# Performance work log

Hardware: AMD Instinct MI355X
Metric: run time of the kernel (lower is better)

## Reference

```python
import jax, jax.numpy as jnp
import numpy as np

N = 50000
IN_C, HID_C, OUT_C = 128, 64, 32
E = 800000
NEG_SLOPE = 0.2


def setup_inputs() -> dict:
    key = jax.random.key(0)
    ks = jax.random.split(key, 8)
    x = jax.random.normal(ks[0], (N, IN_C), dtype=jnp.float32)
    edge_index = jax.random.randint(ks[1], (2, E), 0, N, dtype=jnp.int64)
    # GATConv params (heads=1): lin weight, att_src/att_dst vectors, bias
    sc = 1.0 / np.sqrt(IN_C)
    W = jax.random.uniform(ks[2], (IN_C, HID_C), jnp.float32, -sc, sc)
    att_src = jax.random.normal(ks[3], (HID_C,), jnp.float32) * (1.0 / np.sqrt(HID_C))
    att_dst = jax.random.normal(ks[4], (HID_C,), jnp.float32) * (1.0 / np.sqrt(HID_C))
    bias_conv = jnp.zeros((HID_C,), jnp.float32)
    sl = 1.0 / np.sqrt(HID_C)
    W_lin = jax.random.uniform(ks[5], (HID_C, OUT_C), jnp.float32, -sl, sl)
    b_lin = jax.random.uniform(ks[6], (OUT_C,), jnp.float32, -sl, sl)
    return {"x": x, "edge_index": edge_index, "W": W, "att_src": att_src,
            "att_dst": att_dst, "bias_conv": bias_conv, "W_lin": W_lin, "b_lin": b_lin}


def reference(x, edge_index, W, att_src, att_dst, bias_conv, W_lin, b_lin):
    n = x.shape[0]
    h = x @ W  # [N, HID]
    # add self-loops (PyG GATConv default add_self_loops=True)
    loop = jnp.arange(n, dtype=edge_index.dtype)
    src = jnp.concatenate([edge_index[0], loop])  # [E+N]
    dst = jnp.concatenate([edge_index[1], loop])
    a_src = h @ att_src  # [N]
    a_dst = h @ att_dst
    e = jax.nn.leaky_relu(a_src[src] + a_dst[dst], NEG_SLOPE)  # [E+N]
    # segment softmax over incoming edges per destination node
    m = jax.ops.segment_max(e, dst, num_segments=n)
    e = jnp.exp(e - m[dst])
    denom = jax.ops.segment_sum(e, dst, num_segments=n)
    alpha = e / (denom[dst] + 1e-16)
    msg = alpha[:, None] * h[src]  # [E+N, HID]
    out = jax.ops.segment_sum(msg, dst, num_segments=n) + bias_conv
    out = jax.nn.relu(out)
    return out @ W_lin + b_lin
```

## Files before the change

### kernel.cpp

```cpp
#include <hip/hip_runtime.h>
#include <hip/hip_bf16.h>

#define IN_C  128
#define HID_C 64
#define OUT_C 32
#define NEG_SLOPE 0.2f
#define EPB1    2048
#define EPB2    2048
#define BUCKETW 64
#define RCAP    1536
#define SUPW    1024
#define RCAP1   18432
#define PARTS   9
#define CSTRIDE 16
#define XS_LD   136

typedef short bf16x8 __attribute__((ext_vector_type(8)));
typedef float f32x4  __attribute__((ext_vector_type(4)));

__device__ __forceinline__ unsigned short f2bf(float f) {
    __hip_bfloat16 h = __float2bfloat16(f);
    return *(unsigned short*)&h;
}
__device__ __forceinline__ float bflo(unsigned int u) {
    return __uint_as_float(u << 16);
}
__device__ __forceinline__ float bfhi(unsigned int u) {
    return __uint_as_float(u & 0xffff0000u);
}

__global__ __launch_bounds__(256) void gemm_bin1_kernel(
    const float* __restrict__ x, const float* __restrict__ W,
    const float* __restrict__ att_src, const float* __restrict__ att_dst,
    __hip_bfloat16* __restrict__ hb,
    float* __restrict__ a_src, float* __restrict__ a_dst,
    const int* __restrict__ ei, int E,
    int* __restrict__ bcur1, unsigned* __restrict__ superbuf,
    int ngemm, int n_nodes)
{
    __shared__ __align__(16) unsigned char smem[8960];
    const int t = threadIdx.x;

    if ((int)blockIdx.x < ngemm) {
        unsigned short* xs = (unsigned short*)smem;
        float (*redA)[16] = (float(*)[16])(smem + 4352);
        float (*redD)[16] = (float(*)[16])(smem + 4608);
        const int wv   = t >> 6;
        const int lane = t & 63;
        const int m16  = lane & 15;
        const int quad = lane >> 4;
        const int node0 = blockIdx.x * 16;
        const int nrows = min(16, n_nodes - node0);

        const int ncol = wv * 16 + m16;
        bf16x8 B[4];
#pragma unroll
        for (int k0 = 0; k0 < 4; ++k0)
#pragma unroll
            for (int j = 0; j < 8; ++j)
                B[k0][j] = (short)f2bf(W[(k0 * 32 + quad * 8 + j) * HID_C + ncol]);

        {
            const float4* xg = (const float4*)(x + (long)node0 * IN_C);
#pragma unroll
            for (int i = t; i < 512; i += 256) {
                const int row = i >> 5;
                const int c4  = i & 31;
                float4 v = (row < nrows) ? xg[i] : make_float4(0.f, 0.f, 0.f, 0.f);
                ushort4 u;
                u.x = f2bf(v.x); u.y = f2bf(v.y);
                u.z = f2bf(v.z); u.w = f2bf(v.w);
                *(ushort4*)(xs + row * XS_LD + c4 * 4) = u;
            }
        }
        __syncthreads();

        f32x4 C = {0.f, 0.f, 0.f, 0.f};
#pragma unroll
        for (int k0 = 0; k0 < 4; ++k0) {
            const bf16x8 A = *(const bf16x8*)(xs + m16 * XS_LD + k0 * 32 + quad * 8);
            C = __builtin_amdgcn_mfma_f32_16x16x32_bf16(A, B[k0], C, 0, 0, 0);
        }

#pragma unroll
        for (int r = 0; r < 4; ++r) {
            const int row = quad * 4 + r;
            if (row < nrows)
                hb[(long)(node0 + row) * HID_C + ncol] = __float2bfloat16(C[r]);
        }

        {
            const float av = att_src[ncol];
            const float dv = att_dst[ncol];
            float ps[4], pd[4];
#pragma unroll
            for (int r = 0; r < 4; ++r) { ps[r] = C[r] * av; pd[r] = C[r] * dv; }
#pragma unroll
            for (int off = 1; off <= 8; off <<= 1) {
#pragma unroll
                for (int r = 0; r < 4; ++r) {
                    ps[r] += __shfl_xor(ps[r], off, 64);
                    pd[r] += __shfl_xor(pd[r], off, 64);
                }
            }
            if (m16 == 0) {
#pragma unroll
                for (int r = 0; r < 4; ++r) {
                    redA[wv][quad * 4 + r] = ps[r];
                    redD[wv][quad * 4 + r] = pd[r];
                }
            }
        }
        __syncthreads();
        if (t < 16 && t < nrows) {
            a_src[node0 + t] = redA[0][t] + redA[1][t] + redA[2][t] + redA[3][t];
            a_dst[node0 + t] = redD[0][t] + redD[1][t] + redD[2][t] + redD[3][t];
        }
    } else {
        unsigned* stage = (unsigned*)smem;
        int* excl = (int*)(smem + 8192);
        int* cur  = (int*)(smem + 8448);
        int* gpos = (int*)(smem + 8704);

        const int base = (blockIdx.x - ngemm) * EPB1;
        const int nedge = min(EPB1, E - base);

        if (t < 64) excl[t] = 0;
        __syncthreads();

        for (int i = t; i < nedge; i += 256)
            atomicAdd(&excl[ei[E + base + i] >> 10], 1);
        __syncthreads();

        if (t < 64) {
            int c = excl[t], incl = c;
#pragma unroll
            for (int off = 1; off <= 32; off <<= 1) {
                int u = __shfl_up(incl, off, 64);
                if (t >= off) incl += u;
            }
            excl[t] = incl - c;
            cur[t]  = incl - c;
        }
        __syncthreads();

        for (int i = t; i < nedge; i += 256) {
            const int s = ei[base + i];
            const int d = ei[E + base + i];
            const int sq = d >> 10;
            const int pos = atomicAdd(&cur[sq], 1);
            stage[pos] = (unsigned)s | ((unsigned)(d & 1023) << 16)
                         | ((unsigned)sq << 26);
        }
        __syncthreads();

        if (t < 64) {
            const int c = cur[t] - excl[t];
            gpos[t] = (c > 0) ? atomicAdd(&bcur1[t * CSTRIDE], c) : 0;
        }
        __syncthreads();

        for (int i = t; i < nedge; i += 256) {
            const unsigned r = stage[i];
            const int sq = r >> 26;
            const int dp = gpos[sq] + (i - excl[sq]);
            if (dp < RCAP1) superbuf[(long)sq * RCAP1 + dp] = r;
        }
    }
}

__global__ __launch_bounds__(256) void bin2_kernel(
    const unsigned* __restrict__ superbuf, const int* __restrict__ bcur1,
    int* __restrict__ bcur2, unsigned* __restrict__ bucketbuf)
{
    __shared__ unsigned srt[EPB2];
    __shared__ int cnt[16];
    __shared__ int rp[16];
    __shared__ int cur16[16];
    __shared__ int gpos[16];

    const int t    = threadIdx.x;
    const int sq   = blockIdx.x / PARTS;
    const int part = blockIdx.x % PARTS;
    const int tot  = min(bcur1[sq * CSTRIDE], RCAP1);
    const int beg  = part * EPB2;
    const int n    = min(EPB2, tot - beg);
    if (n <= 0) return;

    if (t < 16) cnt[t] = 0;
    __syncthreads();

    const unsigned* src = superbuf + (long)sq * RCAP1 + beg;

    for (int i = t; i < n; i += 256)
        atomicAdd(&cnt[(src[i] >> 22) & 15], 1);
    __syncthreads();

    if (t == 0) {
        int run = 0;
#pragma unroll
        for (int k = 0; k < 16; ++k) { rp[k] = run; cur16[k] = run; run += cnt[k]; }
    }
    __syncthreads();

    for (int i = t; i < n; i += 256) {
        const unsigned r = src[i];
        const int pos = atomicAdd(&cur16[(r >> 22) & 15], 1);
        srt[pos] = r;
    }
    __syncthreads();

    if (t < 16) {
        const int c = cnt[t];
        const int q2 = sq * 16 + t;
        gpos[t] = (c > 0) ? atomicAdd(&bcur2[q2 * CSTRIDE], c) : 0;
    }
    __syncthreads();

    for (int i = t; i < n; i += 256) {
        const unsigned r = srt[i];
        const int idx = (r >> 22) & 15;
        const int dp  = gpos[idx] + (i - rp[idx]);
        const int q2  = sq * 16 + idx;
        const unsigned nx = (r & 0xFFFFu) | (((r >> 16) & 63u) << 16);
        if (dp < RCAP) bucketbuf[(long)q2 * RCAP + dp] = nx;
    }
}

__global__ __launch_bounds__(512) void bucket_agg_kernel(
    const unsigned* __restrict__ bucketbuf, const int* __restrict__ bcursor,
    const __hip_bfloat16* __restrict__ hb,
    const float* __restrict__ a_src, const float* __restrict__ a_dst,
    const float* __restrict__ bias_conv,
    const float* __restrict__ W_lin, const float* __restrict__ b_lin,
    float* __restrict__ out, int n_nodes)
{
    __shared__ unsigned srtL[RCAP];
    __shared__ int cntd[BUCKETW];
    __shared__ int rp[BUCKETW + 1];
    __shared__ int curd[BUCKETW];

    const int t  = threadIdx.x;
    const int q  = blockIdx.x;
    const int d0 = q * BUCKETW;
    const int dmax = min(BUCKETW, n_nodes - d0);
    const int tot  = min(bcursor[q * CSTRIDE], RCAP);
    const int wv = t >> 6, lane = t & 63, g8 = lane >> 3, l = lane & 7;

    if (t < BUCKETW) cntd[t] = 0;
    __syncthreads();

    const unsigned* gsrc = bucketbuf + (long)q * RCAP;

    for (int i = t; i < tot; i += 512)
        atomicAdd(&cntd[(gsrc[i] >> 16) & 63], 1);
    __syncthreads();

    if (t < 64) {
        int c = cntd[t], incl = c;
#pragma unroll
        for (int off = 1; off <= 32; off <<= 1) {
            int u = __shfl_up(incl, off, 64);
            if (t >= off) incl += u;
        }
        rp[t] = incl - c;
        curd[t] = incl - c;
        if (t == 63) rp[64] = incl;
    }
    __syncthreads();

    for (int i = t; i < tot; i += 512) {
        const unsigned r = gsrc[i];
        const int pos = atomicAdd(&curd[(r >> 16) & 63], 1);
        srtL[pos] = r;
    }
    __syncthreads();

    float Wr[8][4];
#pragma unroll
    for (int kc = 0; kc < 8; ++kc)
#pragma unroll
        for (int kj = 0; kj < 4; ++kj)
            Wr[kc][kj] = W_lin[(l * 8 + kc) * OUT_C + g8 * 4 + kj];
    float biasR[8];
#pragma unroll
    for (int kc = 0; kc < 8; ++kc) biasR[kc] = bias_conv[l * 8 + kc];
    float blinR[4];
#pragma unroll
    for (int kj = 0; kj < 4; ++kj) blinR[kj] = b_lin[g8 * 4 + kj];

    const unsigned short* hbs = (const unsigned short*)hb;

    for (int dloc = wv; dloc < dmax; dloc += 8) {
        const int d = d0 + dloc;
        const float ad = a_dst[d];
        float A[8] = {0.f,0.f,0.f,0.f,0.f,0.f,0.f,0.f};
        float den = 0.f;
        if (g8 == 0) {
            float e = a_src[d] + ad;
            e = (e >= 0.f) ? e : NEG_SLOPE * e;
            const float ws = __expf(e);
            const uint4 hv = *(const uint4*)(hbs + (long)d * HID_C + l * 8);
            den = ws;
            A[0] = ws * bflo(hv.x); A[1] = ws * bfhi(hv.x);
            A[2] = ws * bflo(hv.y); A[3] = ws * bfhi(hv.y);
            A[4] = ws * bflo(hv.z); A[5] = ws * bfhi(hv.z);
            A[6] = ws * bflo(hv.w); A[7] = ws * bfhi(hv.w);
        }
        const int beg = rp[dloc], fin = rp[dloc + 1];
        for (int j = beg + g8; j < fin; j += 16) {
            const int  j1   = j + 8;
            const bool has1 = j1 < fin;
            const unsigned r0 = srtL[j];
            const unsigned r1 = srtL[has1 ? j1 : j];
            const int   s0 = r0 & 0xFFFF;
            const int   s1 = r1 & 0xFFFF;
            const float as0 = a_src[s0];
            const float as1 = a_src[s1];
            const uint4 h0 = *(const uint4*)(hbs + (long)s0 * HID_C + l * 8);
            const uint4 h1 = *(const uint4*)(hbs + (long)s1 * HID_C + l * 8);
            float e0 = as0 + ad; e0 = (e0 >= 0.f) ? e0 : NEG_SLOPE * e0;
            float e1 = as1 + ad; e1 = (e1 >= 0.f) ? e1 : NEG_SLOPE * e1;
            const float w0 = __expf(e0);
            const float w1 = has1 ? __expf(e1) : 0.f;
            den += w0 + w1;
            A[0] = fmaf(w0, bflo(h0.x), A[0]); A[1] = fmaf(w0, bfhi(h0.x), A[1]);
            A[2] = fmaf(w0, bflo(h0.y), A[2]); A[3] = fmaf(w0, bfhi(h0.y), A[3]);
            A[4] = fmaf(w0, bflo(h0.z), A[4]); A[5] = fmaf(w0, bfhi(h0.z), A[5]);
            A[6] = fmaf(w0, bflo(h0.w), A[6]); A[7] = fmaf(w0, bfhi(h0.w), A[7]);
            A[0] = fmaf(w1, bflo(h1.x), A[0]); A[1] = fmaf(w1, bfhi(h1.x), A[1]);
            A[2] = fmaf(w1, bflo(h1.y), A[2]); A[3] = fmaf(w1, bfhi(h1.y), A[3]);
            A[4] = fmaf(w1, bflo(h1.z), A[4]); A[5] = fmaf(w1, bfhi(h1.z), A[5]);
            A[6] = fmaf(w1, bflo(h1.w), A[6]); A[7] = fmaf(w1, bfhi(h1.w), A[7]);
        }
#pragma unroll
        for (int off = 8; off <= 32; off <<= 1) {
#pragma unroll
            for (int k = 0; k < 8; ++k) A[k] += __shfl_xor(A[k], off, 64);
            den += __shfl_xor(den, off, 64);
        }
        const float rd = 1.0f / (den + 1e-16f);
        float p0 = 0.f, p1 = 0.f, p2 = 0.f, p3 = 0.f;
#pragma unroll
        for (int kc = 0; kc < 8; ++kc) {
            float vv = fmaf(A[kc], rd, biasR[kc]);
            vv = vv > 0.f ? vv : 0.f;
            p0 = fmaf(vv, Wr[kc][0], p0);
            p1 = fmaf(vv, Wr[kc][1], p1);
            p2 = fmaf(vv, Wr[kc][2], p2);
            p3 = fmaf(vv, Wr[kc][3], p3);
        }
#pragma unroll
        for (int off = 1; off <= 4; off <<= 1) {
            p0 += __shfl_xor(p0, off, 64);
            p1 += __shfl_xor(p1, off, 64);
            p2 += __shfl_xor(p2, off, 64);
            p3 += __shfl_xor(p3, off, 64);
        }
        if (l == 0) {
            float4 o = make_float4(p0 + blinR[0], p1 + blinR[1],
                                   p2 + blinR[2], p3 + blinR[3]);
            *(float4*)(out + (long)d * OUT_C + g8 * 4) = o;
        }
    }
}

extern "C" void kernel_launch(void* const* d_in, const int* in_sizes, int n_in,
                              void* d_out, int out_size, void* d_ws, size_t ws_size,
                              hipStream_t stream) {
    const float* x         = (const float*)d_in[0];
    const int*   ei        = (const int*)d_in[1];
    const float* W         = (const float*)d_in[2];
    const float* att_src   = (const float*)d_in[3];
    const float* att_dst   = (const float*)d_in[4];
    const float* bias_conv = (const float*)d_in[5];
    const float* W_lin     = (const float*)d_in[6];
    const float* b_lin     = (const float*)d_in[7];
    float*       out       = (float*)d_out;

    const int n_nodes = in_sizes[0] / IN_C;
    const int E       = in_sizes[1] / 2;
    const int B1   = (E + EPB1 - 1) / EPB1;
    const int Q    = (n_nodes + BUCKETW - 1) / BUCKETW;
    const int NSUP = (n_nodes + SUPW - 1) / SUPW;
    const int NG   = (n_nodes + 15) / 16;

    __hip_bfloat16* hb = (__hip_bfloat16*)d_ws;
    float* a_src   = (float*)(hb + (long)n_nodes * HID_C);
    float* a_dst   = a_src + n_nodes;
    int*   bcur1   = (int*)(a_dst + n_nodes);
    int*   bcur2   = bcur1 + NSUP * CSTRIDE;
    unsigned* superbuf  = (unsigned*)(bcur2 + (long)Q * CSTRIDE);
    unsigned* bucketbuf = superbuf + (long)NSUP * RCAP1;

    hipMemsetAsync(bcur1, 0,
                   (size_t)(NSUP + Q) * CSTRIDE * sizeof(int), stream);

    gemm_bin1_kernel<<<NG + B1, 256, 0, stream>>>(
        x, W, att_src, att_dst, hb, a_src, a_dst,
        ei, E, bcur1, superbuf, NG, n_nodes);

    bin2_kernel<<<NSUP * PARTS, 256, 0, stream>>>(
        superbuf, bcur1, bcur2, bucketbuf);

    bucket_agg_kernel<<<Q, 512, 0, stream>>>(
        bucketbuf, bcur2, hb, a_src, a_dst,
        bias_conv, W_lin, b_lin, out, n_nodes);
}
```

Measured before the change: 156.0 us.

## Widen GEMM blocks to 64 rows and interleave two destinations in aggregation

The projection GEMM now processes 64 nodes per block, staging a transposed bf16 copy of W in shared memory and computing per-row attention scores within each wave, which removes the cross-wave reduction and a barrier. The aggregation loop handles two destination nodes per wave simultaneously, issuing four gathers per iteration to raise memory-level parallelism. The costs are larger LDS usage, which may reduce occupancy of the binning blocks in the fused kernel, more registers, and wasted iterations when the two edge lists differ in length.

```diff
diff --git a/kernel.cpp b/kernel.cpp
--- a/kernel.cpp
+++ b/kernel.cpp
@@ -38,32 +38,23 @@
     int* __restrict__ bcur1, unsigned* __restrict__ superbuf,
     int ngemm, int n_nodes)
 {
-    __shared__ __align__(16) unsigned char smem[8960];
+    __shared__ __align__(16) unsigned char smem[34816];
     const int t = threadIdx.x;
 
     if ((int)blockIdx.x < ngemm) {
         unsigned short* xs = (unsigned short*)smem;
-        float (*redA)[16] = (float(*)[16])(smem + 4352);
-        float (*redD)[16] = (float(*)[16])(smem + 4608);
+        unsigned short* wt = (unsigned short*)(smem + 17408);
         const int wv   = t >> 6;
         const int lane = t & 63;
         const int m16  = lane & 15;
         const int quad = lane >> 4;
-        const int node0 = blockIdx.x * 16;
-        const int nrows = min(16, n_nodes - node0);
-
-        const int ncol = wv * 16 + m16;
-        bf16x8 B[4];
-#pragma unroll
-        for (int k0 = 0; k0 < 4; ++k0)
-#pragma unroll
-            for (int j = 0; j < 8; ++j)
-                B[k0][j] = (short)f2bf(W[(k0 * 32 + quad * 8 + j) * HID_C + ncol]);
+        const int node0 = blockIdx.x * 64;
+        const int nrows = min(64, n_nodes - node0);
 
         {
             const float4* xg = (const float4*)(x + (long)node0 * IN_C);
 #pragma unroll
-            for (int i = t; i < 512; i += 256) {
+            for (int i = t; i < 2048; i += 256) {
                 const int row = i >> 5;
                 const int c4  = i & 31;
                 float4 v = (row < nrows) ? xg[i] : make_float4(0.f, 0.f, 0.f, 0.f);
@@ -73,28 +64,60 @@
                 *(ushort4*)(xs + row * XS_LD + c4 * 4) = u;
             }
         }
+        {
+#pragma unroll
+            for (int i = t; i < 2048; i += 256) {
+                const int k  = i >> 4;
+                const int n0 = (i & 15) * 4;
+                const float4 v = *(const float4*)(W + k * HID_C + n0);
+                wt[(n0 + 0) * XS_LD + k] = f2bf(v.x);
+                wt[(n0 + 1) * XS_LD + k] = f2bf(v.y);
+                wt[(n0 + 2) * XS_LD + k] = f2bf(v.z);
+                wt[(n0 + 3) * XS_LD + k] = f2bf(v.w);
+            }
+        }
         __syncthreads();
 
-        f32x4 C = {0.f, 0.f, 0.f, 0.f};
-#pragma unroll
-        for (int k0 = 0; k0 < 4; ++k0) {
-            const bf16x8 A = *(const bf16x8*)(xs + m16 * XS_LD + k0 * 32 + quad * 8);
-            C = __builtin_amdgcn_mfma_f32_16x16x32_bf16(A, B[k0], C, 0, 0, 0);
-        }
-
-#pragma unroll
-        for (int r = 0; r < 4; ++r) {
-            const int row = quad * 4 + r;
-            if (row < nrows)
-                hb[(long)(node0 + row) * HID_C + ncol] = __float2bfloat16(C[r]);
+        const int myrow0 = wv * 16;
+        bf16x8 A[4];
+#pragma unroll
+        for (int k0 = 0; k0 < 4; ++k0)
+            A[k0] = *(const bf16x8*)(xs + (myrow0 + m16) * XS_LD + k0 * 32 + quad * 8);
+
+        f32x4 C[4];
+#pragma unroll
+        for (int c = 0; c < 4; ++c) {
+            C[c] = (f32x4){0.f, 0.f, 0.f, 0.f};
+#pragma unroll
+            for (int k0 = 0; k0 < 4; ++k0) {
+                const bf16x8 B = *(const bf16x8*)(wt + (c * 16 + m16) * XS_LD + k0 * 32 + quad * 8);
+                C[c] = __builtin_amdgcn_mfma_f32_16x16x32_bf16(A[k0], B, C[c], 0, 0, 0);
+            }
+        }
+
+#pragma unroll
+        for (int c = 0; c < 4; ++c) {
+#pragma unroll
+            for (int r = 0; r < 4; ++r) {
+                const int row = myrow0 + quad * 4 + r;
+                if (row < nrows)
+                    hb[(long)(node0 + row) * HID_C + c * 16 + m16] = __float2bfloat16(C[c][r]);
+            }
         }
 
         {
-            const float av = att_src[ncol];
-            const float dv = att_dst[ncol];
-            float ps[4], pd[4];
-#pragma unroll
-            for (int r = 0; r < 4; ++r) { ps[r] = C[r] * av; pd[r] = C[r] * dv; }
+            float ps[4] = {0.f, 0.f, 0.f, 0.f};
+            float pd[4] = {0.f, 0.f, 0.f, 0.f};
+#pragma unroll
+            for (int c = 0; c < 4; ++c) {
+                const float av = att_src[c * 16 + m16];
+                const float dv = att_dst[c * 16 + m16];
+#pragma unroll
+                for (int r = 0; r < 4; ++r) {
+                    ps[r] = fmaf(C[c][r], av, ps[r]);
+                    pd[r] = fmaf(C[c][r], dv, pd[r]);
+                }
+            }
 #pragma unroll
             for (int off = 1; off <= 8; off <<= 1) {
 #pragma unroll
@@ -106,15 +129,13 @@
             if (m16 == 0) {
 #pragma unroll
                 for (int r = 0; r < 4; ++r) {
-                    redA[wv][quad * 4 + r] = ps[r];
-                    redD[wv][quad * 4 + r] = pd[r];
+                    const int row = myrow0 + quad * 4 + r;
+                    if (row < nrows) {
+                        a_src[node0 + row] = ps[r];
+                        a_dst[node0 + row] = pd[r];
+                    }
                 }
             }
-        }
-        __syncthreads();
-        if (t < 16 && t < nrows) {
-            a_src[node0 + t] = redA[0][t] + redA[1][t] + redA[2][t] + redA[3][t];
-            a_dst[node0 + t] = redD[0][t] + redD[1][t] + redD[2][t] + redD[3][t];
         }
     } else {
         unsigned* stage = (unsigned*)smem;
@@ -291,76 +312,156 @@
 
     const unsigned short* hbs = (const unsigned short*)hb;
 
-    for (int dloc = wv; dloc < dmax; dloc += 8) {
-        const int d = d0 + dloc;
-        const float ad = a_dst[d];
-        float A[8] = {0.f,0.f,0.f,0.f,0.f,0.f,0.f,0.f};
-        float den = 0.f;
+    for (int p = 0; p < 4; ++p) {
+        const int dA = wv + p * 16;
+        if (dA >= dmax) break;
+        const int dB = dA + 8;
+        const bool vB = dB < dmax;
+        const int gA = d0 + dA;
+        const int gB = d0 + (vB ? dB : dA);
+        const float adA = a_dst[gA];
+        const float adB = a_dst[gB];
+        float Aa[8] = {0.f,0.f,0.f,0.f,0.f,0.f,0.f,0.f};
+        float Ab[8] = {0.f,0.f,0.f,0.f,0.f,0.f,0.f,0.f};
+        float denA = 0.f, denB = 0.f;
+
         if (g8 == 0) {
-            float e = a_src[d] + ad;
-            e = (e >= 0.f) ? e : NEG_SLOPE * e;
-            const float ws = __expf(e);
-            const uint4 hv = *(const uint4*)(hbs + (long)d * HID_C + l * 8);
-            den = ws;
-            A[0] = ws * bflo(hv.x); A[1] = ws * bfhi(hv.x);
-            A[2] = ws * bflo(hv.y); A[3] = ws * bfhi(hv.y);
-            A[4] = ws * bflo(hv.z); A[5] = ws * bfhi(hv.z);
-            A[6] = ws * bflo(hv.w); A[7] = ws * bfhi(hv.w);
-        }
-        const int beg = rp[dloc], fin = rp[dloc + 1];
-        for (int j = beg + g8; j < fin; j += 16) {
-            const int  j1   = j + 8;
-            const bool has1 = j1 < fin;
-            const unsigned r0 = srtL[j];
-            const unsigned r1 = srtL[has1 ? j1 : j];
-            const int   s0 = r0 & 0xFFFF;
-            const int   s1 = r1 & 0xFFFF;
-            const float as0 = a_src[s0];
-            const float as1 = a_src[s1];
-            const uint4 h0 = *(const uint4*)(hbs + (long)s0 * HID_C + l * 8);
-            const uint4 h1 = *(const uint4*)(hbs + (long)s1 * HID_C + l * 8);
-            float e0 = as0 + ad; e0 = (e0 >= 0.f) ? e0 : NEG_SLOPE * e0;
-            float e1 = as1 + ad; e1 = (e1 >= 0.f) ? e1 : NEG_SLOPE * e1;
-            const float w0 = __expf(e0);
-            const float w1 = has1 ? __expf(e1) : 0.f;
-            den += w0 + w1;
-            A[0] = fmaf(w0, bflo(h0.x), A[0]); A[1] = fmaf(w0, bfhi(h0.x), A[1]);
-            A[2] = fmaf(w0, bflo(h0.y), A[2]); A[3] = fmaf(w0, bfhi(h0.y), A[3]);
-            A[4] = fmaf(w0, bflo(h0.z), A[4]); A[5] = fmaf(w0, bfhi(h0.z), A[5]);
-            A[6] = fmaf(w0, bflo(h0.w), A[6]); A[7] = fmaf(w0, bfhi(h0.w), A[7]);
-            A[0] = fmaf(w1, bflo(h1.x), A[0]); A[1] = fmaf(w1, bfhi(h1.x), A[1]);
-            A[2] = fmaf(w1, bflo(h1.y), A[2]); A[3] = fmaf(w1, bfhi(h1.y), A[3]);
-            A[4] = fmaf(w1, bflo(h1.z), A[4]); A[5] = fmaf(w1, bfhi(h1.z), A[5]);
-            A[6] = fmaf(w1, bflo(h1.w), A[6]); A[7] = fmaf(w1, bfhi(h1.w), A[7]);
-        }
+            {
+                float e = a_src[gA] + adA;
+                e = (e >= 0.f) ? e : NEG_SLOPE * e;
+                const float ws = __expf(e);
+                const uint4 hv = *(const uint4*)(hbs + (long)gA * HID_C + l * 8);
+                denA = ws;
+                Aa[0] = ws * bflo(hv.x); Aa[1] = ws * bfhi(hv.x);
+                Aa[2] = ws * bflo(hv.y); Aa[3] = ws * bfhi(hv.y);
+                Aa[4] = ws * bflo(hv.z); Aa[5] = ws * bfhi(hv.z);
+                Aa[6] = ws * bflo(hv.w); Aa[7] = ws * bfhi(hv.w);
+            }
+            if (vB) {
+                float e = a_src[gB] + adB;
+                e = (e >= 0.f) ? e : NEG_SLOPE * e;
+                const float ws = __expf(e);
+                const uint4 hv = *(const uint4*)(hbs + (long)gB * HID_C + l * 8);
+                denB = ws;
+                Ab[0] = ws * bflo(hv.x); Ab[1] = ws * bfhi(hv.x);
+                Ab[2] = ws * bflo(hv.y); Ab[3] = ws * bfhi(hv.y);
+                Ab[4] = ws * bflo(hv.z); Ab[5] = ws * bfhi(hv.z);
+                Ab[6] = ws * bflo(hv.w); Ab[7] = ws * bfhi(hv.w);
+            }
+        }
+
+        const int begA = rp[dA],            finA = rp[dA + 1];
+        const int begB = vB ? rp[dB] : 0;
+        const int finB = vB ? rp[dB + 1] : 0;
+        int jA = begA + g8, jB = begB + g8;
+
+        while ((jA < finA) | (jB < finB)) {
+            const bool hA0 = jA < finA,       hA1 = (jA + 8) < finA;
+            const bool hB0 = jB < finB,       hB1 = (jB + 8) < finB;
+            const unsigned rA0 = srtL[hA0 ? jA       : 0];
+            const unsigned rA1 = srtL[hA1 ? (jA + 8) : 0];
+            const unsigned rB0 = srtL[hB0 ? jB       : 0];
+            const unsigned rB1 = srtL[hB1 ? (jB + 8) : 0];
+            const int sA0 = rA0 & 0xFFFF, sA1 = rA1 & 0xFFFF;
+            const int sB0 = rB0 & 0xFFFF, sB1 = rB1 & 0xFFFF;
+            const float xA0 = a_src[sA0];
+            const float xA1 = a_src[sA1];
+            const float xB0 = a_src[sB0];
+            const float xB1 = a_src[sB1];
+            const uint4 hA0v = *(const uint4*)(hbs + (long)sA0 * HID_C + l * 8);
+            const uint4 hA1v = *(const uint4*)(hbs + (long)sA1 * HID_C + l * 8);
+            const uint4 hB0v = *(const uint4*)(hbs + (long)sB0 * HID_C + l * 8);
+            const uint4 hB1v = *(const uint4*)(hbs + (long)sB1 * HID_C + l * 8);
+            float e0 = xA0 + adA; e0 = (e0 >= 0.f) ? e0 : NEG_SLOPE * e0;
+            float e1 = xA1 + adA; e1 = (e1 >= 0.f) ? e1 : NEG_SLOPE * e1;
+            float e2 = xB0 + adB; e2 = (e2 >= 0.f) ? e2 : NEG_SLOPE * e2;
+            float e3 = xB1 + adB; e3 = (e3 >= 0.f) ? e3 : NEG_SLOPE * e3;
+            const float wA0 = hA0 ? __expf(e0) : 0.f;
+            const float wA1 = hA1 ? __expf(e1) : 0.f;
+            const float wB0 = hB0 ? __expf(e2) : 0.f;
+            const float wB1 = hB1 ? __expf(e3) : 0.f;
+            denA += wA0 + wA1;
+            denB += wB0 + wB1;
+            Aa[0] = fmaf(wA0, bflo(hA0v.x), Aa[0]); Aa[1] = fmaf(wA0, bfhi(hA0v.x), Aa[1]);
+            Aa[2] = fmaf(wA0, bflo(hA0v.y), Aa[2]); Aa[3] = fmaf(wA0, bfhi(hA0v.y), Aa[3]);
+            Aa[4] = fmaf(wA0, bflo(hA0v.z), Aa[4]); Aa[5] = fmaf(wA0, bfhi(hA0v.z), Aa[5]);
+            Aa[6] = fmaf(wA0, bflo(hA0v.w), Aa[6]); Aa[7] = fmaf(wA0, bfhi(hA0v.w), Aa[7]);
+            Aa[0] = fmaf(wA1, bflo(hA1v.x), Aa[0]); Aa[1] = fmaf(wA1, bfhi(hA1v.x), Aa[1]);
+            Aa[2] = fmaf(wA1, bflo(hA1v.y), Aa[2]); Aa[3] = fmaf(wA1, bfhi(hA1v.y), Aa[3]);
+            Aa[4] = fmaf(wA1, bflo(hA1v.z), Aa[4]); Aa[5] = fmaf(wA1, bfhi(hA1v.z), Aa[5]);
+            Aa[6] = fmaf(wA1, bflo(hA1v.w), Aa[6]); Aa[7] = fmaf(wA1, bfhi(hA1v.w), Aa[7]);
+            Ab[0] = fmaf(wB0, bflo(hB0v.x), Ab[0]); Ab[1] = fmaf(wB0, bfhi(hB0v.x), Ab[1]);
+            Ab[2] = fmaf(wB0, bflo(hB0v.y), Ab[2]); Ab[3] = fmaf(wB0, bfhi(hB0v.y), Ab[3]);
+            Ab[4] = fmaf(wB0, bflo(hB0v.z), Ab[4]); Ab[5] = fmaf(wB0, bfhi(hB0v.z), Ab[5]);
+            Ab[6] = fmaf(wB0, bflo(hB0v.w), Ab[6]); Ab[7] = fmaf(wB0, bfhi(hB0v.w), Ab[7]);
+            Ab[0] = fmaf(wB1, bflo(hB1v.x), Ab[0]); Ab[1] = fmaf(wB1, bfhi(hB1v.x), Ab[1]);
+            Ab[2] = fmaf(wB1, bflo(hB1v.y), Ab[2]); Ab[3] = fmaf(wB1, bfhi(hB1v.y), Ab[3]);
+            Ab[4] = fmaf(wB1, bflo(hB1v.z), Ab[4]); Ab[5] = fmaf(wB1, bfhi(hB1v.z), Ab[5]);
+            Ab[6] = fmaf(wB1, bflo(hB1v.w), Ab[6]); Ab[7] = fmaf(wB1, bfhi(hB1v.w), Ab[7]);
+            jA += 16; jB += 16;
+        }
+
 #pragma unroll
         for (int off = 8; off <= 32; off <<= 1) {
 #pragma unroll
-            for (int k = 0; k < 8; ++k) A[k] += __shfl_xor(A[k], off, 64);
-            den += __shfl_xor(den, off, 64);
-        }
-        const float rd = 1.0f / (den + 1e-16f);
-        float p0 = 0.f, p1 = 0.f, p2 = 0.f, p3 = 0.f;
-#pragma unroll
-        for (int kc = 0; kc < 8; ++kc) {
-            float vv = fmaf(A[kc], rd, biasR[kc]);
-            vv = vv > 0.f ? vv : 0.f;
-            p0 = fmaf(vv, Wr[kc][0], p0);
-            p1 = fmaf(vv, Wr[kc][1], p1);
-            p2 = fmaf(vv, Wr[kc][2], p2);
-            p3 = fmaf(vv, Wr[kc][3], p3);
-        }
-#pragma unroll
-        for (int off = 1; off <= 4; off <<= 1) {
-            p0 += __shfl_xor(p0, off, 64);
-            p1 += __shfl_xor(p1, off, 64);
-            p2 += __shfl_xor(p2, off, 64);
-            p3 += __shfl_xor(p3, off, 64);
-        }
-        if (l == 0) {
-            float4 o = make_float4(p0 + blinR[0], p1 + blinR[1],
-                                   p2 + blinR[2], p3 + blinR[3]);
-            *(float4*)(out + (long)d * OUT_C + g8 * 4) = o;
+            for (int k = 0; k < 8; ++k) Aa[k] += __shfl_xor(Aa[k], off, 64);
+            denA += __shfl_xor(denA, off, 64);
+        }
+        {
+            const float rd = 1.0f / (denA + 1e-16f);
+            float p0 = 0.f, p1 = 0.f, p2 = 0.f, p3 = 0.f;
+#pragma unroll
+            for (int kc = 0; kc < 8; ++kc) {
+                float vv = fmaf(Aa[kc], rd, biasR[kc]);
+                vv = vv > 0.f ? vv : 0.f;
+                p0 = fmaf(vv, Wr[kc][0], p0);
+                p1 = fmaf(vv, Wr[kc][1], p1);
+                p2 = fmaf(vv, Wr[kc][2], p2);
+                p3 = fmaf(vv, Wr[kc][3], p3);
+            }
+#pragma unroll
+            for (int off = 1; off <= 4; off <<= 1) {
+                p0 += __shfl_xor(p0, off, 64);
+                p1 += __shfl_xor(p1, off, 64);
+                p2 += __shfl_xor(p2, off, 64);
+                p3 += __shfl_xor(p3, off, 64);
+            }
+            if (l == 0) {
+                float4 o = make_float4(p0 + blinR[0], p1 + blinR[1],
+                                       p2 + blinR[2], p3 + blinR[3]);
+                *(float4*)(out + (long)gA * OUT_C + g8 * 4) = o;
+            }
+        }
+#pragma unroll
+        for (int off = 8; off <= 32; off <<= 1) {
+#pragma unroll
+            for (int k = 0; k < 8; ++k) Ab[k] += __shfl_xor(Ab[k], off, 64);
+            denB += __shfl_xor(denB, off, 64);
+        }
+        {
+            const float rd = 1.0f / (denB + 1e-16f);
+            float p0 = 0.f, p1 = 0.f, p2 = 0.f, p3 = 0.f;
+#pragma unroll
+            for (int kc = 0; kc < 8; ++kc) {
+                float vv = fmaf(Ab[kc], rd, biasR[kc]);
+                vv = vv > 0.f ? vv : 0.f;
+                p0 = fmaf(vv, Wr[kc][0], p0);
+                p1 = fmaf(vv, Wr[kc][1], p1);
+                p2 = fmaf(vv, Wr[kc][2], p2);
+                p3 = fmaf(vv, Wr[kc][3], p3);
+            }
+#pragma unroll
+            for (int off = 1; off <= 4; off <<= 1) {
+                p0 += __shfl_xor(p0, off, 64);
+                p1 += __shfl_xor(p1, off, 64);
+                p2 += __shfl_xor(p2, off, 64);
+                p3 += __shfl_xor(p3, off, 64);
+            }
+            if (l == 0 && vB) {
+                float4 o = make_float4(p0 + blinR[0], p1 + blinR[1],
+                                       p2 + blinR[2], p3 + blinR[3]);
+                *(float4*)(out + (long)(d0 + dB) * OUT_C + g8 * 4) = o;
+            }
         }
     }
 }
@@ -383,7 +484,7 @@
     const int B1   = (E + EPB1 - 1) / EPB1;
     const int Q    = (n_nodes + BUCKETW - 1) / BUCKETW;
     const int NSUP = (n_nodes + SUPW - 1) / SUPW;
-    const int NG   = (n_nodes + 15) / 16;
+    const int NG   = (n_nodes + 63) / 64;
 
     __hip_bfloat16* hb = (__hip_bfloat16*)d_ws;
     float* a_src   = (float*)(hb + (long)n_nodes * HID_C);
```

Measured after the change: 157.1 us. About the same (+0.7%).

## Drop second binning pass and filter superbuckets directly in aggregation kernel

Applied to the files above, without the earlier changes.

Removes the bin2 kernel and its bucket buffer. Each aggregation block now scans its whole 1024-node superbucket list and keeps the entries whose 32-node sub-bucket matches its own, which shrinks buckets to 32 nodes and blocks to 256 threads. The GEMM part is also restructured so each block handles 64 rows, with W staged transposed in LDS and each wave computing a full 16x64 tile, so the cross-wave reduction for a_src/a_dst is no longer needed. The trade is one fewer launch and one fewer global round trip in exchange for each superbucket being read 32 times by the filtering blocks.

```diff
diff --git a/kernel.cpp b/kernel.cpp
--- a/kernel.cpp
+++ b/kernel.cpp
@@ -6,12 +6,10 @@
 #define OUT_C 32
 #define NEG_SLOPE 0.2f
 #define EPB1    2048
-#define EPB2    2048
-#define BUCKETW 64
-#define RCAP    1536
+#define BUCKETW 32
+#define RCAP    768
 #define SUPW    1024
 #define RCAP1   18432
-#define PARTS   9
 #define CSTRIDE 16
 #define XS_LD   136
 
@@ -38,32 +36,23 @@
     int* __restrict__ bcur1, unsigned* __restrict__ superbuf,
     int ngemm, int n_nodes)
 {
-    __shared__ __align__(16) unsigned char smem[8960];
+    __shared__ __align__(16) unsigned char smem[34816];
     const int t = threadIdx.x;
 
     if ((int)blockIdx.x < ngemm) {
         unsigned short* xs = (unsigned short*)smem;
-        float (*redA)[16] = (float(*)[16])(smem + 4352);
-        float (*redD)[16] = (float(*)[16])(smem + 4608);
+        unsigned short* wt = (unsigned short*)(smem + 17408);
         const int wv   = t >> 6;
         const int lane = t & 63;
         const int m16  = lane & 15;
         const int quad = lane >> 4;
-        const int node0 = blockIdx.x * 16;
-        const int nrows = min(16, n_nodes - node0);
-
-        const int ncol = wv * 16 + m16;
-        bf16x8 B[4];
-#pragma unroll
-        for (int k0 = 0; k0 < 4; ++k0)
-#pragma unroll
-            for (int j = 0; j < 8; ++j)
-                B[k0][j] = (short)f2bf(W[(k0 * 32 + quad * 8 + j) * HID_C + ncol]);
+        const int node0 = blockIdx.x * 64;
+        const int nrows = min(64, n_nodes - node0);
 
         {
             const float4* xg = (const float4*)(x + (long)node0 * IN_C);
 #pragma unroll
-            for (int i = t; i < 512; i += 256) {
+            for (int i = t; i < 2048; i += 256) {
                 const int row = i >> 5;
                 const int c4  = i & 31;
                 float4 v = (row < nrows) ? xg[i] : make_float4(0.f, 0.f, 0.f, 0.f);
@@ -73,28 +62,60 @@
                 *(ushort4*)(xs + row * XS_LD + c4 * 4) = u;
             }
         }
-        __syncthreads();
-
-        f32x4 C = {0.f, 0.f, 0.f, 0.f};
-#pragma unroll
-        for (int k0 = 0; k0 < 4; ++k0) {
-            const bf16x8 A = *(const bf16x8*)(xs + m16 * XS_LD + k0 * 32 + quad * 8);
-            C = __builtin_amdgcn_mfma_f32_16x16x32_bf16(A, B[k0], C, 0, 0, 0);
-        }
-
-#pragma unroll
-        for (int r = 0; r < 4; ++r) {
-            const int row = quad * 4 + r;
-            if (row < nrows)
-                hb[(long)(node0 + row) * HID_C + ncol] = __float2bfloat16(C[r]);
-        }
-
         {
-            const float av = att_src[ncol];
-            const float dv = att_dst[ncol];
-            float ps[4], pd[4];
-#pragma unroll
-            for (int r = 0; r < 4; ++r) { ps[r] = C[r] * av; pd[r] = C[r] * dv; }
+#pragma unroll
+            for (int i = t; i < 2048; i += 256) {
+                const int k  = i >> 4;
+                const int n0 = (i & 15) * 4;
+                const float4 v = *(const float4*)(W + k * HID_C + n0);
+                wt[(n0 + 0) * XS_LD + k] = f2bf(v.x);
+                wt[(n0 + 1) * XS_LD + k] = f2bf(v.y);
+                wt[(n0 + 2) * XS_LD + k] = f2bf(v.z);
+                wt[(n0 + 3) * XS_LD + k] = f2bf(v.w);
+            }
+        }
+        __syncthreads();
+
+        const int myrow0 = wv * 16;
+        bf16x8 A[4];
+#pragma unroll
+        for (int k0 = 0; k0 < 4; ++k0)
+            A[k0] = *(const bf16x8*)(xs + (myrow0 + m16) * XS_LD + k0 * 32 + quad * 8);
+
+        f32x4 C[4];
+#pragma unroll
+        for (int c = 0; c < 4; ++c) {
+            C[c] = (f32x4){0.f, 0.f, 0.f, 0.f};
+#pragma unroll
+            for (int k0 = 0; k0 < 4; ++k0) {
+                const bf16x8 B = *(const bf16x8*)(wt + (c * 16 + m16) * XS_LD + k0 * 32 + quad * 8);
+                C[c] = __builtin_amdgcn_mfma_f32_16x16x32_bf16(A[k0], B, C[c], 0, 0, 0);
+            }
+        }
+
+#pragma unroll
+        for (int c = 0; c < 4; ++c) {
+#pragma unroll
+            for (int r = 0; r < 4; ++r) {
+                const int row = myrow0 + quad * 4 + r;
+                if (row < nrows)
+                    hb[(long)(node0 + row) * HID_C + c * 16 + m16] = __float2bfloat16(C[c][r]);
+            }
+        }
+
+        {
+            float ps[4] = {0.f, 0.f, 0.f, 0.f};
+            float pd[4] = {0.f, 0.f, 0.f, 0.f};
+#pragma unroll
+            for (int c = 0; c < 4; ++c) {
+                const float av = att_src[c * 16 + m16];
+                const float dv = att_dst[c * 16 + m16];
+#pragma unroll
+                for (int r = 0; r < 4; ++r) {
+                    ps[r] = fmaf(C[c][r], av, ps[r]);
+                    pd[r] = fmaf(C[c][r], dv, pd[r]);
+                }
+            }
 #pragma unroll
             for (int off = 1; off <= 8; off <<= 1) {
 #pragma unroll
@@ -106,15 +127,13 @@
             if (m16 == 0) {
 #pragma unroll
                 for (int r = 0; r < 4; ++r) {
-                    redA[wv][quad * 4 + r] = ps[r];
-                    redD[wv][quad * 4 + r] = pd[r];
+                    const int row = myrow0 + quad * 4 + r;
+                    if (row < nrows) {
+                        a_src[node0 + row] = ps[r];
+                        a_dst[node0 + row] = pd[r];
+                    }
                 }
             }
-        }
-        __syncthreads();
-        if (t < 16 && t < nrows) {
-            a_src[node0 + t] = redA[0][t] + redA[1][t] + redA[2][t] + redA[3][t];
-            a_dst[node0 + t] = redD[0][t] + redD[1][t] + redD[2][t] + redD[3][t];
         }
     } else {
         unsigned* stage = (unsigned*)smem;
@@ -169,73 +188,17 @@
     }
 }
 
-__global__ __launch_bounds__(256) void bin2_kernel(
+__global__ __launch_bounds__(256) void agg_kernel(
     const unsigned* __restrict__ superbuf, const int* __restrict__ bcur1,
-    int* __restrict__ bcur2, unsigned* __restrict__ bucketbuf)
-{
-    __shared__ unsigned srt[EPB2];
-    __shared__ int cnt[16];
-    __shared__ int rp[16];
-    __shared__ int cur16[16];
-    __shared__ int gpos[16];
-
-    const int t    = threadIdx.x;
-    const int sq   = blockIdx.x / PARTS;
-    const int part = blockIdx.x % PARTS;
-    const int tot  = min(bcur1[sq * CSTRIDE], RCAP1);
-    const int beg  = part * EPB2;
-    const int n    = min(EPB2, tot - beg);
-    if (n <= 0) return;
-
-    if (t < 16) cnt[t] = 0;
-    __syncthreads();
-
-    const unsigned* src = superbuf + (long)sq * RCAP1 + beg;
-
-    for (int i = t; i < n; i += 256)
-        atomicAdd(&cnt[(src[i] >> 22) & 15], 1);
-    __syncthreads();
-
-    if (t == 0) {
-        int run = 0;
-#pragma unroll
-        for (int k = 0; k < 16; ++k) { rp[k] = run; cur16[k] = run; run += cnt[k]; }
-    }
-    __syncthreads();
-
-    for (int i = t; i < n; i += 256) {
-        const unsigned r = src[i];
-        const int pos = atomicAdd(&cur16[(r >> 22) & 15], 1);
-        srt[pos] = r;
-    }
-    __syncthreads();
-
-    if (t < 16) {
-        const int c = cnt[t];
-        const int q2 = sq * 16 + t;
-        gpos[t] = (c > 0) ? atomicAdd(&bcur2[q2 * CSTRIDE], c) : 0;
-    }
-    __syncthreads();
-
-    for (int i = t; i < n; i += 256) {
-        const unsigned r = srt[i];
-        const int idx = (r >> 22) & 15;
-        const int dp  = gpos[idx] + (i - rp[idx]);
-        const int q2  = sq * 16 + idx;
-        const unsigned nx = (r & 0xFFFFu) | (((r >> 16) & 63u) << 16);
-        if (dp < RCAP) bucketbuf[(long)q2 * RCAP + dp] = nx;
-    }
-}
-
-__global__ __launch_bounds__(512) void bucket_agg_kernel(
-    const unsigned* __restrict__ bucketbuf, const int* __restrict__ bcursor,
     const __hip_bfloat16* __restrict__ hb,
     const float* __restrict__ a_src, const float* __restrict__ a_dst,
     const float* __restrict__ bias_conv,
     const float* __restrict__ W_lin, const float* __restrict__ b_lin,
     float* __restrict__ out, int n_nodes)
 {
+    __shared__ unsigned lst[RCAP];
     __shared__ unsigned srtL[RCAP];
+    __shared__ int lcnt;
     __shared__ int cntd[BUCKETW];
     __shared__ int rp[BUCKETW + 1];
     __shared__ int curd[BUCKETW];
@@ -244,34 +207,54 @@
     const int q  = blockIdx.x;
     const int d0 = q * BUCKETW;
     const int dmax = min(BUCKETW, n_nodes - d0);
-    const int tot  = min(bcursor[q * CSTRIDE], RCAP);
+    const int sq   = q >> 5;
+    const int ridx = q & 31;
+    const int tot1 = min(bcur1[sq * CSTRIDE], RCAP1);
     const int wv = t >> 6, lane = t & 63, g8 = lane >> 3, l = lane & 7;
 
     if (t < BUCKETW) cntd[t] = 0;
+    if (t == 0) lcnt = 0;
     __syncthreads();
 
-    const unsigned* gsrc = bucketbuf + (long)q * RCAP;
-
-    for (int i = t; i < tot; i += 512)
-        atomicAdd(&cntd[(gsrc[i] >> 16) & 63], 1);
+    {
+        const unsigned* sb = superbuf + (long)sq * RCAP1;
+        for (int i0 = t * 4; i0 < tot1; i0 += 1024) {
+            const uint4 v = *(const uint4*)(sb + i0);
+            const unsigned rr[4] = {v.x, v.y, v.z, v.w};
+#pragma unroll
+            for (int k = 0; k < 4; ++k) {
+                const unsigned r = rr[k];
+                const bool ok = (i0 + k < tot1) && ((((r >> 21) ^ (unsigned)ridx) & 31u) == 0u);
+                if (ok) {
+                    const int pos = atomicAdd(&lcnt, 1);
+                    if (pos < RCAP) {
+                        lst[pos] = r & 0x1FFFFFu;
+                        atomicAdd(&cntd[(r >> 16) & 31], 1);
+                    }
+                }
+            }
+        }
+    }
     __syncthreads();
 
-    if (t < 64) {
+    const int nl = min(lcnt, RCAP);
+
+    if (t < 32) {
         int c = cntd[t], incl = c;
 #pragma unroll
-        for (int off = 1; off <= 32; off <<= 1) {
+        for (int off = 1; off <= 16; off <<= 1) {
             int u = __shfl_up(incl, off, 64);
             if (t >= off) incl += u;
         }
         rp[t] = incl - c;
         curd[t] = incl - c;
-        if (t == 63) rp[64] = incl;
+        if (t == 31) rp[32] = incl;
     }
     __syncthreads();
 
-    for (int i = t; i < tot; i += 512) {
-        const unsigned r = gsrc[i];
-        const int pos = atomicAdd(&curd[(r >> 16) & 63], 1);
+    for (int i = t; i < nl; i += 256) {
+        const unsigned r = lst[i];
+        const int pos = atomicAdd(&curd[(r >> 16) & 31], 1);
         srtL[pos] = r;
     }
     __syncthreads();
@@ -291,7 +274,7 @@
 
     const unsigned short* hbs = (const unsigned short*)hb;
 
-    for (int dloc = wv; dloc < dmax; dloc += 8) {
+    for (int dloc = wv; dloc < dmax; dloc += 4) {
         const int d = d0 + dloc;
         const float ad = a_dst[d];
         float A[8] = {0.f,0.f,0.f,0.f,0.f,0.f,0.f,0.f};
@@ -383,27 +366,21 @@
     const int B1   = (E + EPB1 - 1) / EPB1;
     const int Q    = (n_nodes + BUCKETW - 1) / BUCKETW;
     const int NSUP = (n_nodes + SUPW - 1) / SUPW;
-    const int NG   = (n_nodes + 15) / 16;
+    const int NG   = (n_nodes + 63) / 64;
 
     __hip_bfloat16* hb = (__hip_bfloat16*)d_ws;
     float* a_src   = (float*)(hb + (long)n_nodes * HID_C);
     float* a_dst   = a_src + n_nodes;
     int*   bcur1   = (int*)(a_dst + n_nodes);
-    int*   bcur2   = bcur1 + NSUP * CSTRIDE;
-    unsigned* superbuf  = (unsigned*)(bcur2 + (long)Q * CSTRIDE);
-    unsigned* bucketbuf = superbuf + (long)NSUP * RCAP1;
-
-    hipMemsetAsync(bcur1, 0,
-                   (size_t)(NSUP + Q) * CSTRIDE * sizeof(int), stream);
+    unsigned* superbuf = (unsigned*)(bcur1 + (long)NSUP * CSTRIDE);
+
+    hipMemsetAsync(bcur1, 0, (size_t)NSUP * CSTRIDE * sizeof(int), stream);
 
     gemm_bin1_kernel<<<NG + B1, 256, 0, stream>>>(
         x, W, att_src, att_dst, hb, a_src, a_dst,
         ei, E, bcur1, superbuf, NG, n_nodes);
 
-    bin2_kernel<<<NSUP * PARTS, 256, 0, stream>>>(
-        superbuf, bcur1, bcur2, bucketbuf);
-
-    bucket_agg_kernel<<<Q, 512, 0, stream>>>(
-        bucketbuf, bcur2, hb, a_src, a_dst,
+    agg_kernel<<<Q, 256, 0, stream>>>(
+        superbuf, bcur1, hb, a_src, a_dst,
         bias_conv, W_lin, b_lin, out, n_nodes);
 }
```

Measured after the change: 161.8 us. 3.7% more time.
